# Kernel tuning notes

Measured on AMD Instinct MI355X. Metric: run time of the kernel, lower is better.

The kernel has to match this reference:

```python
import jax, jax.numpy as jnp
import numpy as np
from jax import lax

TEMPERATURE = 30.0
PAD = 1  # padding init-kwarg; stride=1, dilation=1


def setup_inputs() -> dict:
    key = jax.random.key(0)
    ks = jax.random.split(key, 8)
    B, D, HID, NF, K, CIN, COUT, HW = 32, 512, 256, 8, 3, 64, 64, 64
    return {
        "filter_condition_input": jax.random.normal(ks[0], (B, D), jnp.float32),
        "model_input": jax.random.normal(ks[1], (B, CIN, HW, HW), jnp.float32),
        "fc1_w": jax.random.normal(ks[2], (HID, D), jnp.float32) * (2.0 / D) ** 0.5,
        "fc1_b": jnp.zeros((HID,), jnp.float32),
        "fc2_w": jax.random.normal(ks[3], (NF, HID), jnp.float32) * (2.0 / HID) ** 0.5,
        "fc2_b": jnp.zeros((NF,), jnp.float32),
        "weight": jax.random.normal(ks[4], (NF, COUT, CIN, K, K), jnp.float32) * 0.05,
        "bias_p": jax.random.normal(ks[5], (NF, COUT), jnp.float32) * 0.05,
    }


def reference(filter_condition_input, model_input, fc1_w, fc1_b, fc2_w, fc2_b, weight, bias_p):
    # Routing MLP -> softmax attention over the num_filters kernel bank
    h = jax.nn.relu(filter_condition_input @ fc1_w.T + fc1_b)
    logits = h @ fc2_w.T + fc2_b
    attn = jax.nn.softmax(logits / TEMPERATURE, axis=1)  # [B, NF]

    # Per-sample aggregated conv kernels and biases
    agg_w = jnp.einsum("bf,foikl->boikl", attn, weight)  # [B, O, Cin, K, K]
    agg_b = attn @ bias_p                                  # [B, O]

    # groups = batch_size grouped conv == independent per-sample conv (vmapped)
    def conv1(x_i, w_i):  # x_i: [Cin,H,W], w_i: [O,Cin,K,K]
        return lax.conv_general_dilated(
            x_i[None], w_i, window_strides=(1, 1),
            padding=((PAD, PAD), (PAD, PAD)),
            dimension_numbers=("NCHW", "OIHW", "NCHW"))[0]

    out = jax.vmap(conv1)(model_input, agg_w) + agg_b[:, :, None, None]  # [B,O,H,W]
    return out, attn
```

## Files before the change

### kernel.cpp

```cpp
#include <hip/hip_runtime.h>
#include <hip/hip_bf16.h>

typedef __hip_bfloat16 bf16;
typedef unsigned short u16;
typedef unsigned int   u32;

#define B_    32
#define D_    512
#define HID_  256
#define NF_   8
#define CIN_  64
#define COUT_ 64
#define HW_   64
#define CONV_OUT_ELEMS (B_ * COUT_ * HW_ * HW_)
#define WBANK_ (NF_ * 36864)

typedef __attribute__((ext_vector_type(8))) short  short8;
typedef __attribute__((ext_vector_type(4))) float  floatx4;

__device__ inline float b2f(bf16 v) { return __bfloat162float(v); }
__device__ inline bf16  f2b(float f) { return __float2bfloat16(f); }
__device__ inline u16 f2bu(float f) { union { bf16 h; u16 u; } c; c.h = __float2bfloat16(f); return c.u; }
__device__ inline float bu2f(u16 u) { union { u32 i; float f; } c; c.i = ((u32)u) << 16; return c.f; }

__device__ inline float ldf(const void* p, int i, int isbf) {
    return isbf ? __bfloat162float(((const bf16*)p)[i]) : ((const float*)p)[i];
}

__device__ inline int word_bf16_sane(u32 v) {
    u32 lo = v & 0xFFFFu;
    u32 ex = (lo >> 7) & 0xFFu;
    return (lo == 0u || (ex >= 64u && ex <= 191u)) ? 1 : 0;
}

__global__ __launch_bounds__(256) void prep_kernel(
    const void* __restrict__ xin,
    const void* __restrict__ x,
    const void* __restrict__ fc1_w,
    const void* __restrict__ fc1_b,
    u16* __restrict__ xin_t,
    float* __restrict__ ws_hs)
{
    __shared__ u16 tr[64][66];
    __shared__ int fl[4];
    const int blk = blockIdx.x;
    const int t = threadIdx.x;

    if (blk < 2048) {
        const int b = blk >> 6, y = blk & 63;
        if (t == 0) fl[0] = 1;
        __syncthreads();
        if (t < 32) {
            u32 w = ((const u32*)xin)[t * 131072];
            if (!word_bf16_sane(w)) atomicAnd(&fl[0], 0);
        }
        __syncthreads();
        const int inbf = fl[0];

        const int ci = t >> 2, xq = (t & 3) * 16;
        u16 vals[16];
        if (inbf) {
            const bf16* src = (const bf16*)xin + (((b * CIN_ + ci) * HW_ + y) * HW_ + xq);
            uint4 v0 = *(const uint4*)src;
            uint4 v1 = *(const uint4*)(src + 8);
            const u32 w8[8] = { v0.x, v0.y, v0.z, v0.w, v1.x, v1.y, v1.z, v1.w };
#pragma unroll
            for (int k = 0; k < 8; ++k) {
                vals[2 * k]     = (u16)(w8[k] & 0xFFFF);
                vals[2 * k + 1] = (u16)(w8[k] >> 16);
            }
        } else {
            const float* src = (const float*)xin + (((b * CIN_ + ci) * HW_ + y) * HW_ + xq);
#pragma unroll
            for (int c = 0; c < 4; ++c) {
                float4 f = *(const float4*)(src + c * 4);
                vals[c * 4 + 0] = f2bu(f.x); vals[c * 4 + 1] = f2bu(f.y);
                vals[c * 4 + 2] = f2bu(f.z); vals[c * 4 + 3] = f2bu(f.w);
            }
        }
#pragma unroll
        for (int k = 0; k < 16; ++k) tr[xq + k][ci] = vals[k];
        __syncthreads();

        const int px = t >> 2, cg = (t & 3) * 16;
        u32 wd[8];
#pragma unroll
        for (int w = 0; w < 8; ++w)
            wd[w] = (u32)tr[px][cg + 2 * w] | ((u32)tr[px][cg + 2 * w + 1] << 16);
        u16* dst = xin_t + (((b * HW_ + y) * HW_ + px) * CIN_ + cg);
        ((uint4*)dst)[0] = make_uint4(wd[0], wd[1], wd[2], wd[3]);
        ((uint4*)dst)[1] = make_uint4(wd[4], wd[5], wd[6], wd[7]);
        return;
    }

    const int h = blk - 2048;
    const int b = t >> 3, seg = t & 7;
    if (t < 3) fl[t] = 1;
    __syncthreads();
    if (t < 96) {
        const int g = t >> 5, k = t & 31;
        const void* buf = (g == 0) ? x : (g == 1) ? fc1_w : fc1_b;
        const int elems = (g == 0) ? B_ * D_ : (g == 1) ? HID_ * D_ : HID_;
        const int nw = elems >> 1;
        const int n = nw < 32 ? nw : 32;
        if (k < n && nw >= 1) {
            u32 v = ((const u32*)buf)[k * (nw / n)];
            if (!word_bf16_sane(v)) atomicAnd(&fl[g], 0);
        }
    }
    __syncthreads();
    const int xbf = fl[0], wbf = fl[1], b1bf = fl[2];

    const int xoff = b * D_ + seg * 64;
    const int woff = h * D_ + seg * 64;
    float p = 0.f;
    if (!xbf && !wbf) {
        float4 xr[16], wr[16];
        const float4* xp = (const float4*)((const float*)x + xoff);
        const float4* wp = (const float4*)((const float*)fc1_w + woff);
#pragma unroll
        for (int c = 0; c < 16; ++c) xr[c] = xp[c];
#pragma unroll
        for (int c = 0; c < 16; ++c) wr[c] = wp[c];
#pragma unroll
        for (int c = 0; c < 16; ++c)
            p += xr[c].x * wr[c].x + xr[c].y * wr[c].y + xr[c].z * wr[c].z + xr[c].w * wr[c].w;
    } else if (xbf && wbf) {
        uint4 xr[8], wr[8];
        const uint4* xp = (const uint4*)((const bf16*)x + xoff);
        const uint4* wp = (const uint4*)((const bf16*)fc1_w + woff);
#pragma unroll
        for (int c = 0; c < 8; ++c) xr[c] = xp[c];
#pragma unroll
        for (int c = 0; c < 8; ++c) wr[c] = wp[c];
#pragma unroll
        for (int c = 0; c < 8; ++c) {
            const u32 xw[4] = { xr[c].x, xr[c].y, xr[c].z, xr[c].w };
            const u32 ww[4] = { wr[c].x, wr[c].y, wr[c].z, wr[c].w };
#pragma unroll
            for (int q2 = 0; q2 < 4; ++q2)
                p += bu2f((u16)(xw[q2] & 0xFFFF)) * bu2f((u16)(ww[q2] & 0xFFFF))
                   + bu2f((u16)(xw[q2] >> 16))    * bu2f((u16)(ww[q2] >> 16));
        }
    } else {
        for (int c = 0; c < 64; ++c) p += ldf(x, xoff + c, xbf) * ldf(fc1_w, woff + c, wbf);
    }
    p += __shfl_xor(p, 1);
    p += __shfl_xor(p, 2);
    p += __shfl_xor(p, 4);
    if (seg == 0) {
        p += ldf(fc1_b, h, b1bf);
        ws_hs[b * HID_ + h] = p > 0.f ? p : 0.f;
    }
}

__global__ __launch_bounds__(256) void fc2_kernel(
    const void* __restrict__ fc2_w,
    const void* __restrict__ fc2_b,
    const void* __restrict__ bias_p,
    const void* __restrict__ xin,
    const float* __restrict__ ws_hs,
    float* __restrict__ ws_attn, float* __restrict__ ws_aggb,
    void* __restrict__ d_out)
{
    __shared__ float hs[HID_];
    __shared__ float at[NF_];
    __shared__ int fl[4];
    const int b = blockIdx.x, t = threadIdx.x;
    if (t < 4) fl[t] = 1;
    hs[t] = ws_hs[b * HID_ + t];
    __syncthreads();
    if (t < 128) {
        const int g = t >> 5, k = t & 31;
        const void* buf = (g == 0) ? fc2_w : (g == 1) ? fc2_b : (g == 2) ? bias_p : xin;
        const int elems = (g == 0) ? NF_ * HID_ : (g == 1) ? NF_ : (g == 2) ? NF_ * COUT_
                                                : B_ * CIN_ * HW_ * HW_;
        const int nw = elems >> 1;
        const int n = nw < 32 ? nw : 32;
        if (k < n && nw >= 1) {
            u32 v = ((const u32*)buf)[k * (nw / n)];
            if (!word_bf16_sane(v)) atomicAnd(&fl[g], 0);
        }
    }
    __syncthreads();
    const int w2bf = fl[0], b2bf = fl[1], bpbf = fl[2], obf = fl[3];

    const int f = t >> 5, j = t & 31;
    const float* hp = hs + j * 8;
    float p;
    if (w2bf) {
        uint4 u = *(const uint4*)((const bf16*)fc2_w + f * HID_ + j * 8);
        p = bu2f((u16)(u.x & 0xFFFF)) * hp[0] + bu2f((u16)(u.x >> 16)) * hp[1]
          + bu2f((u16)(u.y & 0xFFFF)) * hp[2] + bu2f((u16)(u.y >> 16)) * hp[3]
          + bu2f((u16)(u.z & 0xFFFF)) * hp[4] + bu2f((u16)(u.z >> 16)) * hp[5]
          + bu2f((u16)(u.w & 0xFFFF)) * hp[6] + bu2f((u16)(u.w >> 16)) * hp[7];
    } else {
        const float* r = (const float*)fc2_w + f * HID_ + j * 8;
        float4 a = *(const float4*)r, c = *(const float4*)(r + 4);
        p = a.x * hp[0] + a.y * hp[1] + a.z * hp[2] + a.w * hp[3]
          + c.x * hp[4] + c.y * hp[5] + c.z * hp[6] + c.w * hp[7];
    }
#pragma unroll
    for (int m = 16; m; m >>= 1) p += __shfl_xor(p, m);
    if (j == 0) at[f] = (p + ldf(fc2_b, f, b2bf)) * (1.0f / 30.0f);
    __syncthreads();

    if (t == 0) {
        float m = at[0];
#pragma unroll
        for (int ff = 1; ff < NF_; ++ff) m = fmaxf(m, at[ff]);
        float e[NF_], ssum = 0.f;
#pragma unroll
        for (int ff = 0; ff < NF_; ++ff) { e[ff] = __expf(at[ff] - m); ssum += e[ff]; }
        float inv = 1.0f / ssum;
#pragma unroll
        for (int ff = 0; ff < NF_; ++ff) at[ff] = e[ff] * inv;
    }
    __syncthreads();
    if (t < NF_) {
        ws_attn[b * NF_ + t] = at[t];
        if (obf) ((bf16*)d_out)[CONV_OUT_ELEMS + b * NF_ + t] = f2b(at[t]);
        else    ((float*)d_out)[CONV_OUT_ELEMS + b * NF_ + t] = at[t];
    }
    if (t < COUT_) {
        float s = 0.f;
#pragma unroll
        for (int ff = 0; ff < NF_; ++ff) s += at[ff] * ldf(bias_p, ff * COUT_ + t, bpbf);
        ws_aggb[b * COUT_ + t] = s;
    }
}

__global__ __launch_bounds__(256) void agg_kernel(
    const void* __restrict__ weight,
    const float* __restrict__ ws_attn,
    u16* __restrict__ aggw)
{
    __shared__ float lds[2304];
    __shared__ float s_at[NF_];
    __shared__ int   s_wbf;
    const int t  = threadIdx.x;
    const int b  = blockIdx.x >> 4;
    const int o0 = (blockIdx.x & 15) * 4;

    if (t == 0) s_wbf = 1;
    if (t < NF_) s_at[t] = ws_attn[b * NF_ + t];
    __syncthreads();
    if (t < 32) {
        const int nw = WBANK_ >> 1, step = nw / 32;
        u32 v = ((const u32*)weight)[t * step];
        if (!word_bf16_sane(v)) atomicAnd(&s_wbf, 0);
    }
    __syncthreads();
    const int wbf = s_wbf;

#pragma unroll
    for (int j = 0; j < 9; ++j) {
        const int flat = t + 256 * j;
        const int o_l = flat / 576, rr = flat - o_l * 576;
        const int gbase = (o0 + o_l) * 576 + rr;
        float s = 0.f;
        if (wbf) {
#pragma unroll
            for (int f = 0; f < NF_; ++f) s += s_at[f] * b2f(((const bf16*)weight)[f * 36864 + gbase]);
        } else {
#pragma unroll
            for (int f = 0; f < NF_; ++f) s += s_at[f] * ((const float*)weight)[f * 36864 + gbase];
        }
        lds[flat] = s;
    }
    __syncthreads();
#pragma unroll
    for (int j = 0; j < 9; ++j) {
        const int e = t + 256 * j;
        const int tap = e >> 8, o_l = (e >> 6) & 3, ci = e & 63;
        aggw[b * 36864 + tap * 4096 + (o0 + o_l) * 64 + ci] = f2bu(lds[o_l * 576 + ci * 9 + tap]);
    }
}

__global__ __launch_bounds__(256) void conv_mfma2(
    const u16*  __restrict__ xin_t,
    const u16*  __restrict__ aggw,
    const float* __restrict__ aggb,
    const void* __restrict__ xin,
    void* __restrict__ out)
{
    __shared__ u16 out_s[4 * 64 * 68];
    __shared__ float bias_s[COUT_];
    __shared__ int s_ok;

    const int t    = threadIdx.x;
    const int bz   = blockIdx.x;
    const int b    = bz >> 4;
    const int y0   = (bz & 15) * 4;
    const int wv   = t >> 6;
    const int lane = t & 63, l15 = lane & 15, q = lane >> 4;

    if (t == 0) s_ok = 1;
    __syncthreads();
    if (t < 32) {
        u32 w = ((const u32*)xin)[t * 131072];
        if (!word_bf16_sane(w)) atomicAnd(&s_ok, 0);
    }
    if (t < COUT_) bias_s[t] = aggb[b * COUT_ + t];
    __syncthreads();
    const int outbf = s_ok;

    floatx4 acc[4][4];
#pragma unroll
    for (int mt = 0; mt < 4; ++mt)
#pragma unroll
        for (int nt = 0; nt < 4; ++nt) acc[mt][nt] = (floatx4)0.f;

    const u16* Abase = aggw + b * 36864;
    const int laneA = l15 * 64 + q * 8;
    const int laneB = l15 * 64 + q * 8;

#pragma unroll
    for (int kh = 0; kh < 3; ++kh) {
        const int gy = y0 + wv + kh - 1;
        if (gy >= 0 && gy < HW_) {
            const u16* Brow = xin_t + (b * HW_ + gy) * (HW_ * CIN_);
#pragma unroll
            for (int kw = 0; kw < 3; ++kw) {
                const u16* Atap = Abase + (kh * 3 + kw) * 4096;
#pragma unroll
                for (int ks = 0; ks < 2; ++ks) {
                    short8 af[4], bf[4];
#pragma unroll
                    for (int mt = 0; mt < 4; ++mt)
                        af[mt] = *(const short8*)(Atap + mt * 1024 + ks * 32 + laneA);
#pragma unroll
                    for (int nt = 0; nt < 4; ++nt) {
                        const int col = nt * 16 + l15 + kw - 1;
                        if (col >= 0 && col < HW_)
                            bf[nt] = *(const short8*)(Brow + col * 64 + ks * 32 + q * 8);
                        else
                            bf[nt] = (short8)0;
                    }
#pragma unroll
                    for (int mt = 0; mt < 4; ++mt)
#pragma unroll
                        for (int nt = 0; nt < 4; ++nt)
                            acc[mt][nt] = __builtin_amdgcn_mfma_f32_16x16x32_bf16(
                                af[mt], bf[nt], acc[mt][nt], 0, 0, 0);
                }
            }
        }
    }

#pragma unroll
    for (int mt = 0; mt < 4; ++mt) {
        floatx4 bb = *(const floatx4*)&bias_s[mt * 16 + q * 4];
#pragma unroll
        for (int nt = 0; nt < 4; ++nt) {
#pragma unroll
            for (int rg = 0; rg < 4; ++rg) {
                const float v = acc[mt][nt][rg] + bb[rg];
                out_s[(wv * 64 + (mt * 16 + q * 4 + rg)) * 68 + nt * 16 + l15] = f2bu(v);
            }
        }
    }
    __syncthreads();
#pragma unroll
    for (int j = 0; j < 16; ++j) {
        const int c = t + 256 * j;
        const int x0 = (c & 15) * 4, o = (c >> 4) & 63, w2 = c >> 10;
        const u16* src = &out_s[(w2 * 64 + o) * 68 + x0];
        const u16 h0 = src[0], h1 = src[1], h2 = src[2], h3 = src[3];
        const int gidx = ((b * COUT_ + o) * HW_ + (y0 + w2)) * HW_ + x0;
        if (outbf) {
            uint2 pk; pk.x = (u32)h0 | ((u32)h1 << 16); pk.y = (u32)h2 | ((u32)h3 << 16);
            *(uint2*)((u16*)out + gidx) = pk;
        } else {
            float4 f; f.x = bu2f(h0); f.y = bu2f(h1); f.z = bu2f(h2); f.w = bu2f(h3);
            *(float4*)((float*)out + gidx) = f;
        }
    }
}

extern "C" void kernel_launch(void* const* d_in, const int* in_sizes, int n_in,
                              void* d_out, int out_size, void* d_ws, size_t ws_size,
                              hipStream_t stream) {
    const void* x      = d_in[0];
    const void* xin    = d_in[1];
    const void* fc1_w  = d_in[2];
    const void* fc1_b  = d_in[3];
    const void* fc2_w  = d_in[4];
    const void* fc2_b  = d_in[5];
    const void* weight = d_in[6];
    const void* bias_p = d_in[7];

    float* ws      = (float*)d_ws;
    float* ws_attn = ws;
    float* ws_aggb = ws + 256;
    float* ws_hs   = ws + 2304;
    u16*   ws_aggw = (u16*)(ws + 10496);
    u16*   ws_xint = (u16*)(ws + 600320);

    prep_kernel<<<dim3(2048 + HID_), dim3(256), 0, stream>>>(
        xin, x, fc1_w, fc1_b, ws_xint, ws_hs);

    fc2_kernel<<<dim3(B_), dim3(256), 0, stream>>>(
        fc2_w, fc2_b, bias_p, xin, ws_hs, ws_attn, ws_aggb, d_out);

    agg_kernel<<<dim3(B_ * 16), dim3(256), 0, stream>>>(weight, ws_attn, ws_aggw);

    conv_mfma2<<<dim3(B_ * 16), dim3(256), 0, stream>>>(
        ws_xint, ws_aggw, ws_aggb, xin, d_out);
}
```

Before: 157.2 us.

## Stage input halo rows in LDS for conv MFMA B operand

Each conv block now cooperatively loads its 6 input rows (4 output rows plus halo) with zero-padded borders into padded shared memory, then reads the B fragments from LDS instead of global memory with per-lane bounds checks. This removes redundant global loads across the three kh and kw taps and the boundary branching. Shared memory grows to about 57KB, which may lower occupancy, and an extra barrier is added before the output staging reuses the buffer.

```diff
diff --git a/kernel.cpp b/kernel.cpp
--- a/kernel.cpp
+++ b/kernel.cpp
@@ -277,14 +277,14 @@
     }
 }
 
-__global__ __launch_bounds__(256) void conv_mfma2(
+__global__ __launch_bounds__(256) void conv_mfma3(
     const u16*  __restrict__ xin_t,
     const u16*  __restrict__ aggw,
     const float* __restrict__ aggb,
     const void* __restrict__ xin,
     void* __restrict__ out)
 {
-    __shared__ u16 out_s[4 * 64 * 68];
+    __shared__ __align__(16) u16 smem[28512];
     __shared__ float bias_s[COUT_];
     __shared__ int s_ok;
 
@@ -302,6 +302,21 @@
         if (!word_bf16_sane(w)) atomicAnd(&s_ok, 0);
     }
     if (t < COUT_) bias_s[t] = aggb[b * COUT_ + t];
+
+#pragma unroll
+    for (int j = 0; j < 12; ++j) {
+        const int item = t + 256 * j;
+        const int cg = item & 7, colm = (item >> 3) & 63, r = item >> 9;
+        const int gy = y0 - 1 + r;
+        uint4 v = make_uint4(0, 0, 0, 0);
+        if (gy >= 0 && gy < HW_)
+            v = *(const uint4*)(xin_t + (((b * HW_ + gy) * HW_ + colm) * CIN_ + cg * 8));
+        *(uint4*)&smem[(r * 66 + colm + 1) * 72 + cg * 8] = v;
+    }
+    if (t < 96) {
+        const int cg = t & 7, c = (t >> 3) & 1, r = t >> 4;
+        *(uint4*)&smem[(r * 66 + c * 65) * 72 + cg * 8] = make_uint4(0, 0, 0, 0);
+    }
     __syncthreads();
     const int outbf = s_ok;
 
@@ -313,13 +328,11 @@
 
     const u16* Abase = aggw + b * 36864;
     const int laneA = l15 * 64 + q * 8;
-    const int laneB = l15 * 64 + q * 8;
 
 #pragma unroll
     for (int kh = 0; kh < 3; ++kh) {
         const int gy = y0 + wv + kh - 1;
         if (gy >= 0 && gy < HW_) {
-            const u16* Brow = xin_t + (b * HW_ + gy) * (HW_ * CIN_);
 #pragma unroll
             for (int kw = 0; kw < 3; ++kw) {
                 const u16* Atap = Abase + (kh * 3 + kw) * 4096;
@@ -330,13 +343,9 @@
                     for (int mt = 0; mt < 4; ++mt)
                         af[mt] = *(const short8*)(Atap + mt * 1024 + ks * 32 + laneA);
 #pragma unroll
-                    for (int nt = 0; nt < 4; ++nt) {
-                        const int col = nt * 16 + l15 + kw - 1;
-                        if (col >= 0 && col < HW_)
-                            bf[nt] = *(const short8*)(Brow + col * 64 + ks * 32 + q * 8);
-                        else
-                            bf[nt] = (short8)0;
-                    }
+                    for (int nt = 0; nt < 4; ++nt)
+                        bf[nt] = *(const short8*)&smem[((wv + kh) * 66 + nt * 16 + l15 + kw) * 72
+                                                       + ks * 32 + q * 8];
 #pragma unroll
                     for (int mt = 0; mt < 4; ++mt)
 #pragma unroll
@@ -348,6 +357,8 @@
         }
     }
 
+    __syncthreads();
+    u16* out_s = smem;
 #pragma unroll
     for (int mt = 0; mt < 4; ++mt) {
         floatx4 bb = *(const floatx4*)&bias_s[mt * 16 + q * 4];
@@ -405,6 +416,6 @@
 
     agg_kernel<<<dim3(B_ * 16), dim3(256), 0, stream>>>(weight, ws_attn, ws_aggw);
 
-    conv_mfma2<<<dim3(B_ * 16), dim3(256), 0, stream>>>(
+    conv_mfma3<<<dim3(B_ * 16), dim3(256), 0, stream>>>(
         ws_xint, ws_aggw, ws_aggb, xin, d_out);
 }
```

Result: faster. 147.2 us (-6.3%).

## Fuse fc2 into aggregation kernel and stage conv operands in LDS

Applied to the files above, without the earlier changes.

Merges the fc2/softmax kernel into the per-sample weight aggregation kernel. Each of the 16 blocks per sample recomputes the small fc2 and softmax itself, which removes one launch and the attention round-trip through the workspace. The conv kernel now stages aggregated weights and a padded input halo in shared memory, in two 32-channel phases, instead of loading MFMA operands straight from global memory. The halo tile handles the padding and lets neighbouring taps and rows reuse the same data, at the cost of more shared memory per block (lower occupancy) and extra barriers.

```diff
diff --git a/kernel.cpp b/kernel.cpp
--- a/kernel.cpp
+++ b/kernel.cpp
@@ -154,27 +154,34 @@
     }
 }
 
-__global__ __launch_bounds__(256) void fc2_kernel(
+__global__ __launch_bounds__(256) void agg2_kernel(
+    const void* __restrict__ weight,
     const void* __restrict__ fc2_w,
     const void* __restrict__ fc2_b,
     const void* __restrict__ bias_p,
     const void* __restrict__ xin,
     const float* __restrict__ ws_hs,
-    float* __restrict__ ws_attn, float* __restrict__ ws_aggb,
+    float* __restrict__ ws_aggb,
+    u16* __restrict__ aggw,
     void* __restrict__ d_out)
 {
+    __shared__ float lds[2304];
     __shared__ float hs[HID_];
     __shared__ float at[NF_];
-    __shared__ int fl[4];
-    const int b = blockIdx.x, t = threadIdx.x;
-    if (t < 4) fl[t] = 1;
+    __shared__ int   fl[5];
+    const int t  = threadIdx.x;
+    const int b  = blockIdx.x >> 4;
+    const int o0 = (blockIdx.x & 15) * 4;
+
+    if (t < 5) fl[t] = 1;
     hs[t] = ws_hs[b * HID_ + t];
     __syncthreads();
-    if (t < 128) {
+    if (t < 160) {
         const int g = t >> 5, k = t & 31;
-        const void* buf = (g == 0) ? fc2_w : (g == 1) ? fc2_b : (g == 2) ? bias_p : xin;
+        const void* buf = (g == 0) ? fc2_w : (g == 1) ? fc2_b : (g == 2) ? bias_p
+                        : (g == 3) ? xin : weight;
         const int elems = (g == 0) ? NF_ * HID_ : (g == 1) ? NF_ : (g == 2) ? NF_ * COUT_
-                                                : B_ * CIN_ * HW_ * HW_;
+                        : (g == 3) ? B_ * CIN_ * HW_ * HW_ : WBANK_;
         const int nw = elems >> 1;
         const int n = nw < 32 ? nw : 32;
         if (k < n && nw >= 1) {
@@ -183,28 +190,29 @@
         }
     }
     __syncthreads();
-    const int w2bf = fl[0], b2bf = fl[1], bpbf = fl[2], obf = fl[3];
-
-    const int f = t >> 5, j = t & 31;
-    const float* hp = hs + j * 8;
-    float p;
-    if (w2bf) {
-        uint4 u = *(const uint4*)((const bf16*)fc2_w + f * HID_ + j * 8);
-        p = bu2f((u16)(u.x & 0xFFFF)) * hp[0] + bu2f((u16)(u.x >> 16)) * hp[1]
-          + bu2f((u16)(u.y & 0xFFFF)) * hp[2] + bu2f((u16)(u.y >> 16)) * hp[3]
-          + bu2f((u16)(u.z & 0xFFFF)) * hp[4] + bu2f((u16)(u.z >> 16)) * hp[5]
-          + bu2f((u16)(u.w & 0xFFFF)) * hp[6] + bu2f((u16)(u.w >> 16)) * hp[7];
-    } else {
-        const float* r = (const float*)fc2_w + f * HID_ + j * 8;
-        float4 a = *(const float4*)r, c = *(const float4*)(r + 4);
-        p = a.x * hp[0] + a.y * hp[1] + a.z * hp[2] + a.w * hp[3]
-          + c.x * hp[4] + c.y * hp[5] + c.z * hp[6] + c.w * hp[7];
-    }
-#pragma unroll
-    for (int m = 16; m; m >>= 1) p += __shfl_xor(p, m);
-    if (j == 0) at[f] = (p + ldf(fc2_b, f, b2bf)) * (1.0f / 30.0f);
-    __syncthreads();
-
+    const int w2bf = fl[0], b2bf = fl[1], bpbf = fl[2], obf = fl[3], wbf = fl[4];
+
+    {
+        const int f = t >> 5, j = t & 31;
+        const float* hp = hs + j * 8;
+        float p;
+        if (w2bf) {
+            uint4 u = *(const uint4*)((const bf16*)fc2_w + f * HID_ + j * 8);
+            p = bu2f((u16)(u.x & 0xFFFF)) * hp[0] + bu2f((u16)(u.x >> 16)) * hp[1]
+              + bu2f((u16)(u.y & 0xFFFF)) * hp[2] + bu2f((u16)(u.y >> 16)) * hp[3]
+              + bu2f((u16)(u.z & 0xFFFF)) * hp[4] + bu2f((u16)(u.z >> 16)) * hp[5]
+              + bu2f((u16)(u.w & 0xFFFF)) * hp[6] + bu2f((u16)(u.w >> 16)) * hp[7];
+        } else {
+            const float* r = (const float*)fc2_w + f * HID_ + j * 8;
+            float4 a = *(const float4*)r, c = *(const float4*)(r + 4);
+            p = a.x * hp[0] + a.y * hp[1] + a.z * hp[2] + a.w * hp[3]
+              + c.x * hp[4] + c.y * hp[5] + c.z * hp[6] + c.w * hp[7];
+        }
+#pragma unroll
+        for (int m = 16; m; m >>= 1) p += __shfl_xor(p, m);
+        if (j == 0) at[f] = (p + ldf(fc2_b, f, b2bf)) * (1.0f / 30.0f);
+    }
+    __syncthreads();
     if (t == 0) {
         float m = at[0];
 #pragma unroll
@@ -217,41 +225,18 @@
         for (int ff = 0; ff < NF_; ++ff) at[ff] = e[ff] * inv;
     }
     __syncthreads();
-    if (t < NF_) {
-        ws_attn[b * NF_ + t] = at[t];
+
+    if ((blockIdx.x & 15) == 0 && t < NF_) {
         if (obf) ((bf16*)d_out)[CONV_OUT_ELEMS + b * NF_ + t] = f2b(at[t]);
         else    ((float*)d_out)[CONV_OUT_ELEMS + b * NF_ + t] = at[t];
     }
-    if (t < COUT_) {
+    if (t < 4) {
+        const int o = o0 + t;
         float s = 0.f;
 #pragma unroll
-        for (int ff = 0; ff < NF_; ++ff) s += at[ff] * ldf(bias_p, ff * COUT_ + t, bpbf);
-        ws_aggb[b * COUT_ + t] = s;
-    }
-}
-
-__global__ __launch_bounds__(256) void agg_kernel(
-    const void* __restrict__ weight,
-    const float* __restrict__ ws_attn,
-    u16* __restrict__ aggw)
-{
-    __shared__ float lds[2304];
-    __shared__ float s_at[NF_];
-    __shared__ int   s_wbf;
-    const int t  = threadIdx.x;
-    const int b  = blockIdx.x >> 4;
-    const int o0 = (blockIdx.x & 15) * 4;
-
-    if (t == 0) s_wbf = 1;
-    if (t < NF_) s_at[t] = ws_attn[b * NF_ + t];
-    __syncthreads();
-    if (t < 32) {
-        const int nw = WBANK_ >> 1, step = nw / 32;
-        u32 v = ((const u32*)weight)[t * step];
-        if (!word_bf16_sane(v)) atomicAnd(&s_wbf, 0);
-    }
-    __syncthreads();
-    const int wbf = s_wbf;
+        for (int ff = 0; ff < NF_; ++ff) s += at[ff] * ldf(bias_p, ff * COUT_ + o, bpbf);
+        ws_aggb[b * COUT_ + o] = s;
+    }
 
 #pragma unroll
     for (int j = 0; j < 9; ++j) {
@@ -261,10 +246,10 @@
         float s = 0.f;
         if (wbf) {
 #pragma unroll
-            for (int f = 0; f < NF_; ++f) s += s_at[f] * b2f(((const bf16*)weight)[f * 36864 + gbase]);
+            for (int f = 0; f < NF_; ++f) s += at[f] * b2f(((const bf16*)weight)[f * 36864 + gbase]);
         } else {
 #pragma unroll
-            for (int f = 0; f < NF_; ++f) s += s_at[f] * ((const float*)weight)[f * 36864 + gbase];
+            for (int f = 0; f < NF_; ++f) s += at[f] * ((const float*)weight)[f * 36864 + gbase];
         }
         lds[flat] = s;
     }
@@ -277,16 +262,18 @@
     }
 }
 
-__global__ __launch_bounds__(256) void conv_mfma2(
+__global__ __launch_bounds__(256) void conv_mfma4(
     const u16*  __restrict__ xin_t,
     const u16*  __restrict__ aggw,
     const float* __restrict__ aggb,
     const void* __restrict__ xin,
     void* __restrict__ out)
 {
-    __shared__ u16 out_s[4 * 64 * 68];
+    __shared__ __align__(16) u16 smem[38880];
     __shared__ float bias_s[COUT_];
     __shared__ int s_ok;
+    u16* A_s = smem;
+    u16* B_s = smem + 23040;
 
     const int t    = threadIdx.x;
     const int bz   = blockIdx.x;
@@ -312,42 +299,50 @@
         for (int nt = 0; nt < 4; ++nt) acc[mt][nt] = (floatx4)0.f;
 
     const u16* Abase = aggw + b * 36864;
-    const int laneA = l15 * 64 + q * 8;
-    const int laneB = l15 * 64 + q * 8;
-
-#pragma unroll
-    for (int kh = 0; kh < 3; ++kh) {
-        const int gy = y0 + wv + kh - 1;
-        if (gy >= 0 && gy < HW_) {
-            const u16* Brow = xin_t + (b * HW_ + gy) * (HW_ * CIN_);
-#pragma unroll
-            for (int kw = 0; kw < 3; ++kw) {
-                const u16* Atap = Abase + (kh * 3 + kw) * 4096;
-#pragma unroll
-                for (int ks = 0; ks < 2; ++ks) {
-                    short8 af[4], bf[4];
-#pragma unroll
-                    for (int mt = 0; mt < 4; ++mt)
-                        af[mt] = *(const short8*)(Atap + mt * 1024 + ks * 32 + laneA);
-#pragma unroll
-                    for (int nt = 0; nt < 4; ++nt) {
-                        const int col = nt * 16 + l15 + kw - 1;
-                        if (col >= 0 && col < HW_)
-                            bf[nt] = *(const short8*)(Brow + col * 64 + ks * 32 + q * 8);
-                        else
-                            bf[nt] = (short8)0;
-                    }
-#pragma unroll
-                    for (int mt = 0; mt < 4; ++mt)
-#pragma unroll
-                        for (int nt = 0; nt < 4; ++nt)
-                            acc[mt][nt] = __builtin_amdgcn_mfma_f32_16x16x32_bf16(
-                                af[mt], bf[nt], acc[mt][nt], 0, 0, 0);
-                }
+
+    for (int ph = 0; ph < 2; ++ph) {
+        const int ci0 = ph * 32;
+#pragma unroll
+        for (int j = 0; j < 9; ++j) {
+            const int item = t + 256 * j;
+            const int cg = item & 3, o = (item >> 2) & 63, tap = item >> 8;
+            uint4 v = *(const uint4*)(Abase + tap * 4096 + o * 64 + ci0 + cg * 8);
+            *(uint4*)&A_s[tap * 2560 + o * 40 + cg * 8] = v;
+        }
+#pragma unroll
+        for (int j = 0; j < 7; ++j) {
+            const int item = t + 256 * j;
+            if (item < 1584) {
+                const int cg = item & 3, col = (item >> 2) % 66, r = item / 264;
+                const int gy = y0 - 1 + r, gx = col - 1;
+                uint4 v = make_uint4(0, 0, 0, 0);
+                if (gy >= 0 && gy < HW_ && gx >= 0 && gx < HW_)
+                    v = *(const uint4*)(xin_t + (((b * HW_ + gy) * HW_ + gx) * CIN_ + ci0 + cg * 8));
+                *(uint4*)&B_s[r * 2640 + col * 40 + cg * 8] = v;
             }
         }
-    }
-
+        __syncthreads();
+#pragma unroll
+        for (int tap = 0; tap < 9; ++tap) {
+            const int kh = tap / 3, kw = tap % 3;
+            short8 af[4], bf[4];
+#pragma unroll
+            for (int mt = 0; mt < 4; ++mt)
+                af[mt] = *(const short8*)&A_s[tap * 2560 + (mt * 16 + l15) * 40 + q * 8];
+#pragma unroll
+            for (int nt = 0; nt < 4; ++nt)
+                bf[nt] = *(const short8*)&B_s[(wv + kh) * 2640 + (nt * 16 + l15 + kw) * 40 + q * 8];
+#pragma unroll
+            for (int mt = 0; mt < 4; ++mt)
+#pragma unroll
+                for (int nt = 0; nt < 4; ++nt)
+                    acc[mt][nt] = __builtin_amdgcn_mfma_f32_16x16x32_bf16(
+                        af[mt], bf[nt], acc[mt][nt], 0, 0, 0);
+        }
+        __syncthreads();
+    }
+
+    u16* out_s = smem;
 #pragma unroll
     for (int mt = 0; mt < 4; ++mt) {
         floatx4 bb = *(const floatx4*)&bias_s[mt * 16 + q * 4];
@@ -391,7 +386,6 @@
     const void* bias_p = d_in[7];
 
     float* ws      = (float*)d_ws;
-    float* ws_attn = ws;
     float* ws_aggb = ws + 256;
     float* ws_hs   = ws + 2304;
     u16*   ws_aggw = (u16*)(ws + 10496);
@@ -400,11 +394,9 @@
     prep_kernel<<<dim3(2048 + HID_), dim3(256), 0, stream>>>(
         xin, x, fc1_w, fc1_b, ws_xint, ws_hs);
 
-    fc2_kernel<<<dim3(B_), dim3(256), 0, stream>>>(
-        fc2_w, fc2_b, bias_p, xin, ws_hs, ws_attn, ws_aggb, d_out);
-
-    agg_kernel<<<dim3(B_ * 16), dim3(256), 0, stream>>>(weight, ws_attn, ws_aggw);
-
-    conv_mfma2<<<dim3(B_ * 16), dim3(256), 0, stream>>>(
+    agg2_kernel<<<dim3(B_ * 16), dim3(256), 0, stream>>>(
+        weight, fc2_w, fc2_b, bias_p, xin, ws_hs, ws_aggb, ws_aggw, d_out);
+
+    conv_mfma4<<<dim3(B_ * 16), dim3(256), 0, stream>>>(
         ws_xint, ws_aggw, ws_aggb, xin, d_out);
 }
```

Measured after the change: 138.8 us. -11.7%, faster.
